# Optimization experiments

Measured on AMD Instinct MI355X. Metric: run time of the kernel, lower is better.

The kernel has to match this reference:

```python
import jax, jax.numpy as jnp
import numpy as np

B, T, C = 2, 2048, 1024
H, DH = 16, 64  # num_heads, dim_head; inner_dim = H*DH = C


def setup_inputs() -> dict:
    key = jax.random.key(0)
    k_x, k_q, k_k, k_v, k_o, k_r = jax.random.split(key, 6)
    scaled = lambda k, shape, fan: (jax.random.normal(k, shape, jnp.float32) / np.sqrt(fan).astype(np.float32))
    x = jax.random.normal(k_x, (B, T, C), jnp.float32)
    Wq = scaled(k_q, (C, H * DH), C)
    Wk = scaled(k_k, (C, H * DH), C)
    Wv = scaled(k_v, (C, H * DH), C)
    Wo = scaled(k_o, (H * DH, C), H * DH)
    bo = jnp.zeros((C,), jnp.float32)
    # learned relative position bias table, indexed by (i - j) in [-(T-1), T-1]
    rel_table = jax.random.normal(k_r, (H, 2 * T - 1), jnp.float32) * 0.02
    # causal mask, broadcast over batch and heads
    mask = jnp.tril(jnp.ones((T, T), bool))[None, None]  # [1,1,T,T]
    return {"x": x, "Wq": Wq, "Wk": Wk, "Wv": Wv, "Wo": Wo, "bo": bo,
            "rel_table": rel_table, "mask": mask}


def reference(x, Wq, Wk, Wv, Wo, bo, rel_table, mask):
    Bx, Tx, Cx = x.shape
    split = lambda t: t.reshape(Bx, Tx, H, DH).transpose(0, 2, 1, 3)  # [B,H,T,DH]
    q = split(x @ Wq) * (DH ** -0.5)
    k = split(x @ Wk)
    v = split(x @ Wv)
    # relative position bias: bias[h,i,j] = rel_table[h, i-j + T-1]
    rel_idx = jnp.arange(Tx)[:, None] - jnp.arange(Tx)[None, :] + (Tx - 1)  # [T,T]
    bias = rel_table[:, rel_idx]  # [H,T,T]
    score = jnp.einsum('bhid,bhjd->bhij', q, k) + bias[None]
    mask_value = -jnp.finfo(score.dtype).max
    score = jnp.where(mask, score, mask_value)
    attn = jax.nn.softmax(score, axis=-1)
    y = jnp.einsum('bhij,bhjd->bhid', attn, v)
    y = y.transpose(0, 2, 1, 3).reshape(Bx, Tx, H * DH)
    return y @ Wo + bo
```

## Files before the change

kernel.cpp:

```cpp
#include <hip/hip_runtime.h>
#include <hip/hip_bf16.h>
#include <stdint.h>


#define T_SEQ 2048
#define NH    16
#define DHD   64
#define CDIM  1024

typedef unsigned short u16;
typedef unsigned int   u32;
typedef __attribute__((ext_vector_type(8))) __bf16 bf16x8;
typedef __attribute__((ext_vector_type(4))) float f32x4;

#define WAITL0   asm volatile("s_waitcnt lgkmcnt(0)" ::: "memory")

__device__ __forceinline__ float bf2f(u16 b){
  union { u32 u; float f; } v; v.u = ((u32)b) << 16; return v.f;
}
__device__ __forceinline__ u16 f2bf(float f){
  union { __bf16 h; u16 u; } v; v.h = (__bf16)f;
  return v.u;
}

__device__ __forceinline__ void gload_lds16(const u16* g, u16* l){
  __builtin_amdgcn_global_load_lds(
      (const __attribute__((address_space(1))) void*)g,
      (__attribute__((address_space(3))) void*)l, 16, 0, 0);
}

__device__ __forceinline__ uint4 load8(const void* p, long elem, int isbf){
  if (isbf) return *(const uint4*)((const u16*)p + elem);
  const float* fp = (const float*)p + elem;
  float4 a = *(const float4*)fp, b = *(const float4*)(fp + 4);
  uint4 r;
  r.x = (u32)f2bf(a.x) | ((u32)f2bf(a.y) << 16);
  r.y = (u32)f2bf(a.z) | ((u32)f2bf(a.w) << 16);
  r.z = (u32)f2bf(b.x) | ((u32)f2bf(b.y) << 16);
  r.w = (u32)f2bf(b.z) | ((u32)f2bf(b.w) << 16);
  return r;
}
__device__ __forceinline__ float loadf(const void* p, long idx, int isbf){
  return isbf ? bf2f(((const u16*)p)[idx]) : ((const float*)p)[idx];
}

__global__ __launch_bounds__(256) void classify(const u32* __restrict__ x,
                                                int* __restrict__ flag){
  __shared__ int cnt[256];
  int c = 0;
#pragma unroll
  for (int i = 0; i < 16; i++){
    u32 w = x[threadIdx.x * 16 + i];
    int e = (w >> 7) & 0xFF;
    c += (e >= 110 && e <= 140);
  }
  cnt[threadIdx.x] = c;
  __syncthreads();
  for (int s = 128; s > 0; s >>= 1){
    if ((int)threadIdx.x < s) cnt[threadIdx.x] += cnt[threadIdx.x + s];
    __syncthreads();
  }
  if (threadIdx.x == 0) *flag = (cnt[0] > 2048) ? 1 : 0;
}

__global__ __launch_bounds__(256) void prep(
    const void* __restrict__ w0, const void* __restrict__ w1,
    const void* __restrict__ w2,
    u16* __restrict__ o0, u16* __restrict__ o1, u16* __restrict__ o2,
    const void* __restrict__ x, u16* __restrict__ xbf,
    const int* __restrict__ flag)
{
  __shared__ u16 tile[64][72];
  const int isbf = *flag;
  const int bid = (int)blockIdx.x;
  const int tid = threadIdx.x;

  if (bid >= 768){
    const long i = ((long)(bid - 768) * 256 + tid) * 8;
    *(uint4*)(xbf + i) = load8(x, i, isbf);
    return;
  }

  const int z = bid >> 8;
  const void* in = z==0 ? w0 : z==1 ? w1 : w2;
  u16*      out  = z==0 ? o0 : z==1 ? o1 : o2;
  const int r0 = ((bid >> 4) & 15) * 64, c0 = (bid & 15) * 64;
  const int rr = tid >> 3;
  const int cc = (tid & 7) * 8;
#pragma unroll
  for (int rd = 0; rd < 2; rd++){
    int r = rd*32 + rr;
    *(uint4*)&tile[r][cc] = load8(in, (long)(r0 + r)*CDIM + c0 + cc, isbf);
  }
  __syncthreads();
#pragma unroll
  for (int rd = 0; rd < 2; rd++){
    int oc = rd*32 + rr;
    uint4 wv; u32* wp = (u32*)&wv;
#pragma unroll
    for (int t = 0; t < 4; t++){
      u32 lo = tile[cc + 2*t][oc];
      u32 hi = tile[cc + 2*t + 1][oc];
      wp[t] = lo | (hi << 16);
    }
    *(uint4*)(out + (long)(c0 + oc)*CDIM + r0 + cc) = wv;
  }
}

__global__ __launch_bounds__(256) void transposeW(
    const void* __restrict__ w0, const void* __restrict__ w1,
    const void* __restrict__ w2,
    u16* __restrict__ o0, u16* __restrict__ o1, u16* __restrict__ o2,
    const int* __restrict__ flag)
{
  __shared__ u16 tile[64][72];
  const int isbf = *flag;
  const int z = blockIdx.z;
  const void* in = z==0 ? w0 : z==1 ? w1 : w2;
  u16*      out  = z==0 ? o0 : z==1 ? o1 : o2;
  const int tid = threadIdx.x;
  const int r0 = blockIdx.y * 64, c0 = blockIdx.x * 64;
  const int rr = tid >> 3;
  const int cc = (tid & 7) * 8;
#pragma unroll
  for (int rd = 0; rd < 2; rd++){
    int r = rd*32 + rr;
    *(uint4*)&tile[r][cc] = load8(in, (long)(r0 + r)*CDIM + c0 + cc, isbf);
  }
  __syncthreads();
#pragma unroll
  for (int rd = 0; rd < 2; rd++){
    int oc = rd*32 + rr;
    uint4 wv; u32* wp = (u32*)&wv;
#pragma unroll
    for (int t = 0; t < 4; t++){
      u32 lo = tile[cc + 2*t][oc];
      u32 hi = tile[cc + 2*t + 1][oc];
      wp[t] = lo | (hi << 16);
    }
    *(uint4*)(out + (long)(c0 + oc)*CDIM + r0 + cc) = wv;
  }
}

__device__ __forceinline__ void gemm_body(
    const u16* __restrict__ A, const u16* __restrict__ BT,
    const void* __restrict__ bias, void* __restrict__ out,
    float scale, int mode, int m0, int n0, int io_isbf)
{
  __shared__ u16 ldsA[2][128*32];
  __shared__ u16 ldsB[2][128*32];
  const int tid = threadIdx.x;
  const int wid = tid >> 6, lane = tid & 63;
  const int col = lane & 15, quad = lane >> 4;
  const int wm = (wid >> 1) * 64, wn = (wid & 1) * 64;

  const int c0 = wid*128 + lane, c1 = c0 + 64;
  const int r0c = c0 >> 2, g0c = c0 & 3;
  const int r1c = c1 >> 2, g1c = c1 & 3;
  const long aoff0 = (long)r0c*CDIM + ((g0c ^ (r0c & 3)) << 3);
  const long aoff1 = (long)r1c*CDIM + ((g1c ^ (r1c & 3)) << 3);
  const int lds0 = (wid*128)*8;
  const int lds1 = (wid*128 + 64)*8;

  const u16* gA = A  + (long)m0*CDIM;
  const u16* gB = BT + (long)n0*CDIM;

  auto stage = [&](int buf, int k0){
    gload_lds16(gA + k0 + aoff0, &ldsA[buf][lds0]);
    gload_lds16(gA + k0 + aoff1, &ldsA[buf][lds1]);
    gload_lds16(gB + k0 + aoff0, &ldsB[buf][lds0]);
    gload_lds16(gB + k0 + aoff1, &ldsB[buf][lds1]);
  };

  f32x4 acc[4][4] = {};
  const int NK = CDIM / 32;

  stage(0, 0);
  __syncthreads();

  int cur = 0;
  for (int k = 0; k < NK; k++){
    if (k + 1 < NK) stage(cur ^ 1, (k + 1) * 32);

    bf16x8 af[4], bfr[4];
#pragma unroll
    for (int mi = 0; mi < 4; mi++){
      const int r = wm + mi*16 + col;
      af[mi] = *(const bf16x8*)&ldsA[cur][r*32 + ((quad ^ (r & 3)) * 8)];
    }
#pragma unroll
    for (int ni = 0; ni < 4; ni++){
      const int r = wn + ni*16 + col;
      bfr[ni] = *(const bf16x8*)&ldsB[cur][r*32 + ((quad ^ (r & 3)) * 8)];
    }
#pragma unroll
    for (int mi = 0; mi < 4; mi++)
#pragma unroll
      for (int ni = 0; ni < 4; ni++)
        acc[mi][ni] = __builtin_amdgcn_mfma_f32_16x16x32_bf16(af[mi], bfr[ni], acc[mi][ni], 0, 0, 0);

    __syncthreads();
    cur ^= 1;
  }

  if (mode == 2){
#pragma unroll
    for (int ni = 0; ni < 4; ni++){
      const int n = n0 + wn + ni*16 + col;
      const int h = n >> 6, d = n & 63;
#pragma unroll
      for (int mi = 0; mi < 4; mi++){
        const int m = m0 + wm + mi*16 + quad*4;
        const int b = m >> 11, t = m & (T_SEQ-1);
        uint2 pk;
        pk.x = (u32)f2bf(acc[mi][ni][0]) | ((u32)f2bf(acc[mi][ni][1]) << 16);
        pk.y = (u32)f2bf(acc[mi][ni][2]) | ((u32)f2bf(acc[mi][ni][3]) << 16);
        *(uint2*)((u16*)out + ((long)(b*NH + h)*DHD + d)*T_SEQ + t) = pk;
      }
    }
  } else {
#pragma unroll
    for (int ni = 0; ni < 4; ni++){
      const int n = n0 + wn + ni*16 + col;
      const float bv = bias ? loadf(bias, n, io_isbf) : 0.f;
#pragma unroll
      for (int mi = 0; mi < 4; mi++){
#pragma unroll
        for (int r = 0; r < 4; r++){
          const int m = m0 + wm + mi*16 + quad*4 + r;
          const float v = acc[mi][ni][r] * scale + bv;
          if (mode == 0){
            const long idx = (long)m*CDIM + n;
            if (io_isbf) ((u16*)out)[idx] = f2bf(v);
            else         ((float*)out)[idx] = v;
          } else {
            const int b = m >> 11, t = m & (T_SEQ-1), h = n >> 6, d = n & 63;
            ((u16*)out)[((long)(b*NH + h)*T_SEQ + t)*DHD + d] = f2bf(v);
          }
        }
      }
    }
  }
}

__global__ __launch_bounds__(256) void gemm_qkv(
    const u16* __restrict__ xbf,
    const u16* __restrict__ WqT, const u16* __restrict__ WkT, const u16* __restrict__ WvT,
    u16* __restrict__ Qb, u16* __restrict__ Kb, u16* __restrict__ VTb)
{
  const int z = blockIdx.z;
  const u16* BT = z==0 ? WqT : z==1 ? WkT : WvT;
  u16*      dst = z==0 ? Qb  : z==1 ? Kb  : VTb;
  const float scale = (z==0) ? 0.125f * 1.44269504f : 1.0f;
  const int mode = (z==2) ? 2 : 1;
  gemm_body(xbf, BT, nullptr, dst, scale, mode, blockIdx.x*128, blockIdx.y*128, 1);
}

__global__ __launch_bounds__(256) void gemm_out(
    const u16* __restrict__ Y, const u16* __restrict__ WoT,
    const void* __restrict__ bo, void* __restrict__ out,
    const int* __restrict__ flag)
{
  gemm_body(Y, WoT, bo, out, 1.0f, 0, blockIdx.x*128, blockIdx.y*128, *flag);
}

__global__ __launch_bounds__(256) void attn64(
    const u16* __restrict__ Q, const u16* __restrict__ K, const u16* __restrict__ VT,
    const void* __restrict__ rel, u16* __restrict__ Y,
    const int* __restrict__ flag)
{
  __shared__ u16 ldsK[2][64*64];
  __shared__ u16 ldsV[2][64*64];
  __shared__ u16 ldsP[4][16*88];
  __shared__ float ldsBias[2112];

  const int isbf = *flag;
  const int tid = threadIdx.x, wid = tid >> 6, lane = tid & 63;
  const int col = lane & 15, quad = lane >> 4;

  const int l = (int)blockIdx.x;
  const int xcd = l & 7, s = l >> 3;
  const int bh = xcd * 4 + (s & 3);
  const int g = s >> 2, gq = g >> 3, g0 = g & 7;
  const int ti = (gq == 0) ? 31 - g0
               : (gq == 1) ? g0
               : (gq == 2) ? 23 - g0
                           : 8 + g0;
  const int i0 = ti * 64;

  const int h = bh & (NH - 1);
  const int b = bh >> 4;

  const u16* Qh = Q  + (long)bh * T_SEQ * DHD;
  const u16* Kh = K  + (long)bh * T_SEQ * DHD;
  const u16* Vh = VT + (long)bh * DHD * T_SEQ;
  const long relbase = (long)h * (2*T_SEQ - 1) + (T_SEQ - 1);
  const float MLOG = 16.0f * 1.44269504f;

  const int srow0 = wid*8 + (lane >> 3);
  const int srow1 = srow0 + 32;
  const int soff  = ((lane & 7) ^ ((lane >> 3) & 7)) * 8;
  const int sb0   = wid*512;
  const int sb1   = 2048 + wid*512;

  auto stage = [&](int buf, int j0){
    gload_lds16(Kh + (long)(j0 + srow0)*DHD + soff, &ldsK[buf][sb0]);
    gload_lds16(Kh + (long)(j0 + srow1)*DHD + soff, &ldsK[buf][sb1]);
    gload_lds16(Vh + (long)srow0*T_SEQ + j0 + soff, &ldsV[buf][sb0]);
    gload_lds16(Vh + (long)srow1*T_SEQ + j0 + soff, &ldsV[buf][sb1]);
  };

  const int nbias = i0 + 127;
  for (int t = tid; t < nbias; t += 256)
    ldsBias[t] = loadf(rel, relbase + t - 63, isbf) * 1.44269504f - MLOG;

  bf16x8 qf0, qf1;
  {
    const u16* qp = Qh + (long)(i0 + wid*16 + col)*DHD + quad*8;
    qf0 = *(const bf16x8*)qp;
    qf1 = *(const bf16x8*)(qp + 32);
  }

  f32x4 O[4] = {};
  float lsumv = 0.f;
  const int icol = i0 + wid*16 + col;
  const int irow = i0 + wid*16 + quad*4;

  stage(0, 0);
  __syncthreads();

  int cur = 0;
  for (int j0 = 0; j0 <= i0; j0 += 64){
    const bool have_next = (j0 + 64 <= i0);
    if (have_next) stage(cur ^ 1, j0 + 64);

    f32x4 sv[4] = {};
#pragma unroll
    for (int kb = 0; kb < 2; kb++){
#pragma unroll
      for (int nb = 0; nb < 4; nb++){
        const int row = nb*16 + col;
        const int sl = ((kb*4 + quad) ^ (row & 7)) * 8;
        bf16x8 kf = *(const bf16x8*)&ldsK[cur][row*64 + sl];
        sv[nb] = __builtin_amdgcn_mfma_f32_16x16x32_bf16(kf, kb ? qf1 : qf0, sv[nb], 0, 0, 0);
      }
    }

    const bool diag = (j0 == i0);
#pragma unroll
    for (int nb = 0; nb < 4; nb++){
      const float* bp = &ldsBias[icol - j0 - nb*16 - quad*4 + 63];
#pragma unroll
      for (int r = 0; r < 4; r++){
        float arg = sv[nb][r] + bp[-r];
        if (diag && (nb*16 + quad*4 + r > wid*16 + col)) arg = -1e9f;
        float p;
        asm volatile("v_exp_f32 %0, %1" : "=v"(p) : "v"(arg));
        sv[nb][r] = p;
        lsumv += p;
      }
    }

    u16* Pw = ldsP[wid];
#pragma unroll
    for (int nb = 0; nb < 4; nb++){
      u32 lo, hi;
      asm("v_cvt_pk_bf16_f32 %0, %1, %2" : "=v"(lo) : "v"(sv[nb][0]), "v"(sv[nb][1]));
      asm("v_cvt_pk_bf16_f32 %0, %1, %2" : "=v"(hi) : "v"(sv[nb][2]), "v"(sv[nb][3]));
      uint2 pk; pk.x = lo; pk.y = hi;
      *(uint2*)&Pw[col*88 + nb*16 + quad*4] = pk;
    }
    WAITL0;

#pragma unroll
    for (int kb = 0; kb < 2; kb++){
      bf16x8 pf = *(const bf16x8*)&Pw[col*88 + kb*32 + quad*8];
#pragma unroll
      for (int nb = 0; nb < 4; nb++){
        const int row = nb*16 + col;
        const int sl = ((kb*4 + quad) ^ (row & 7)) * 8;
        bf16x8 vf = *(const bf16x8*)&ldsV[cur][row*64 + sl];
        O[nb] = __builtin_amdgcn_mfma_f32_16x16x32_bf16(pf, vf, O[nb], 0, 0, 0);
      }
    }

    __syncthreads();
    cur ^= 1;
  }

  lsumv += __shfl_xor(lsumv, 16, 64);
  lsumv += __shfl_xor(lsumv, 32, 64);
  float rs[4];
#pragma unroll
  for (int r = 0; r < 4; r++)
    rs[r] = __shfl(lsumv, quad*4 + r, 16);

#pragma unroll
  for (int nb = 0; nb < 4; nb++){
#pragma unroll
    for (int r = 0; r < 4; r++){
      const int i = irow + r;
      const int d = nb*16 + col;
      Y[((long)(b*T_SEQ + i))*CDIM + h*DHD + d] = f2bf(O[nb][r] / rs[r]);
    }
  }
}

extern "C" void kernel_launch(void* const* d_in, const int* in_sizes, int n_in,
                              void* d_out, int out_size, void* d_ws, size_t ws_size,
                              hipStream_t stream)
{
  (void)in_sizes; (void)n_in; (void)out_size; (void)ws_size;
  const void* x   = d_in[0];
  const void* Wq  = d_in[1];
  const void* Wk  = d_in[2];
  const void* Wv  = d_in[3];
  const void* Wo  = d_in[4];
  const void* bo  = d_in[5];
  const void* rel = d_in[6];

  char* ws = (char*)d_ws;
  const size_t MB = 1024*1024;
  int* flag = (int*)ws;
  char* base = ws + 256;
  u16* WqT = (u16*)(base + 0*MB);
  u16* WkT = (u16*)(base + 2*MB);
  u16* WvT = (u16*)(base + 4*MB);
  u16* Kb  = (u16*)(base + 6*MB);
  u16* VTb = (u16*)(base + 14*MB);
  u16* Yb  = (u16*)(base + 0*MB);
  u16* WoT = (u16*)(base + 8*MB);
  u16* Qb  = (u16*)d_out;
  u16* xbf = Qb + 4u*1024*1024;

  dim3 blk(256);
  classify  <<<1, blk, 0, stream>>>((const u32*)x, flag);
  prep      <<<dim3(2816), blk, 0, stream>>>(Wq, Wk, Wv, WqT, WkT, WvT, x, xbf, flag);
  gemm_qkv  <<<dim3(32,8,3),  blk, 0, stream>>>(xbf, WqT, WkT, WvT, Qb, Kb, VTb);
  attn64    <<<dim3(1024),  blk, 0, stream>>>(Qb, Kb, VTb, rel, Yb, flag);
  transposeW<<<dim3(16,16,1), blk, 0, stream>>>(Wo, Wo, Wo, WoT, WoT, WoT, flag);
  gemm_out  <<<dim3(32,8),    blk, 0, stream>>>(Yb, WoT, bo, d_out, flag);
}
```

Baseline: 214.7 us.

## Inline dtype sniffing per block and fuse Wo transpose with output GEMM cooperatively

```diff
diff --git a/kernel.cpp b/kernel.cpp
--- a/kernel.cpp
+++ b/kernel.cpp
@@ -1,5 +1,6 @@
 #include <hip/hip_runtime.h>
 #include <hip/hip_bf16.h>
+#include <hip/hip_cooperative_groups.h>
 #include <stdint.h>
 
 
@@ -21,6 +22,18 @@
 __device__ __forceinline__ u16 f2bf(float f){
   union { __bf16 h; u16 u; } v; v.h = (__bf16)f;
   return v.u;
+}
+
+__device__ __forceinline__ int sniff_bf16(const void* xp){
+  __shared__ int sflag;
+  if (threadIdx.x < 64){
+    u32 w = ((const u32*)xp)[threadIdx.x * 64];
+    int e = (w >> 7) & 0xFF;
+    unsigned long long m = __ballot(e >= 110 && e <= 140);
+    if (threadIdx.x == 0) sflag = (__popcll(m) > 32) ? 1 : 0;
+  }
+  __syncthreads();
+  return sflag;
 }
 
 __device__ __forceinline__ void gload_lds16(const u16* g, u16* l){
@@ -44,34 +57,14 @@
   return isbf ? bf2f(((const u16*)p)[idx]) : ((const float*)p)[idx];
 }
 
-__global__ __launch_bounds__(256) void classify(const u32* __restrict__ x,
-                                                int* __restrict__ flag){
-  __shared__ int cnt[256];
-  int c = 0;
-#pragma unroll
-  for (int i = 0; i < 16; i++){
-    u32 w = x[threadIdx.x * 16 + i];
-    int e = (w >> 7) & 0xFF;
-    c += (e >= 110 && e <= 140);
-  }
-  cnt[threadIdx.x] = c;
-  __syncthreads();
-  for (int s = 128; s > 0; s >>= 1){
-    if ((int)threadIdx.x < s) cnt[threadIdx.x] += cnt[threadIdx.x + s];
-    __syncthreads();
-  }
-  if (threadIdx.x == 0) *flag = (cnt[0] > 2048) ? 1 : 0;
-}
-
 __global__ __launch_bounds__(256) void prep(
     const void* __restrict__ w0, const void* __restrict__ w1,
     const void* __restrict__ w2,
     u16* __restrict__ o0, u16* __restrict__ o1, u16* __restrict__ o2,
-    const void* __restrict__ x, u16* __restrict__ xbf,
-    const int* __restrict__ flag)
+    const void* __restrict__ x, u16* __restrict__ xbf)
 {
   __shared__ u16 tile[64][72];
-  const int isbf = *flag;
+  const int isbf = sniff_bf16(x);
   const int bid = (int)blockIdx.x;
   const int tid = threadIdx.x;
 
@@ -85,41 +78,6 @@
   const void* in = z==0 ? w0 : z==1 ? w1 : w2;
   u16*      out  = z==0 ? o0 : z==1 ? o1 : o2;
   const int r0 = ((bid >> 4) & 15) * 64, c0 = (bid & 15) * 64;
-  const int rr = tid >> 3;
-  const int cc = (tid & 7) * 8;
-#pragma unroll
-  for (int rd = 0; rd < 2; rd++){
-    int r = rd*32 + rr;
-    *(uint4*)&tile[r][cc] = load8(in, (long)(r0 + r)*CDIM + c0 + cc, isbf);
-  }
-  __syncthreads();
-#pragma unroll
-  for (int rd = 0; rd < 2; rd++){
-    int oc = rd*32 + rr;
-    uint4 wv; u32* wp = (u32*)&wv;
-#pragma unroll
-    for (int t = 0; t < 4; t++){
-      u32 lo = tile[cc + 2*t][oc];
-      u32 hi = tile[cc + 2*t + 1][oc];
-      wp[t] = lo | (hi << 16);
-    }
-    *(uint4*)(out + (long)(c0 + oc)*CDIM + r0 + cc) = wv;
-  }
-}
-
-__global__ __launch_bounds__(256) void transposeW(
-    const void* __restrict__ w0, const void* __restrict__ w1,
-    const void* __restrict__ w2,
-    u16* __restrict__ o0, u16* __restrict__ o1, u16* __restrict__ o2,
-    const int* __restrict__ flag)
-{
-  __shared__ u16 tile[64][72];
-  const int isbf = *flag;
-  const int z = blockIdx.z;
-  const void* in = z==0 ? w0 : z==1 ? w1 : w2;
-  u16*      out  = z==0 ? o0 : z==1 ? o1 : o2;
-  const int tid = threadIdx.x;
-  const int r0 = blockIdx.y * 64, c0 = blockIdx.x * 64;
   const int rr = tid >> 3;
   const int cc = (tid & 7) * 8;
 #pragma unroll
@@ -256,25 +214,57 @@
   gemm_body(xbf, BT, nullptr, dst, scale, mode, blockIdx.x*128, blockIdx.y*128, 1);
 }
 
-__global__ __launch_bounds__(256) void gemm_out(
-    const u16* __restrict__ Y, const u16* __restrict__ WoT,
-    const void* __restrict__ bo, void* __restrict__ out,
-    const int* __restrict__ flag)
-{
-  gemm_body(Y, WoT, bo, out, 1.0f, 0, blockIdx.x*128, blockIdx.y*128, *flag);
+__global__ __launch_bounds__(256) void out_fused(
+    const void* __restrict__ Wo, u16* __restrict__ WoT,
+    const u16* __restrict__ Y, const void* __restrict__ bo,
+    void* __restrict__ outp, const void* __restrict__ xs)
+{
+  const int isbf = sniff_bf16(xs);
+  const int bid = (int)blockIdx.x;
+  const int tid = threadIdx.x;
+
+  {
+    __shared__ u16 tile[64][72];
+    const int r0 = (bid >> 4) * 64, c0 = (bid & 15) * 64;
+    const int rr = tid >> 3;
+    const int cc = (tid & 7) * 8;
+#pragma unroll
+    for (int rd = 0; rd < 2; rd++){
+      int r = rd*32 + rr;
+      *(uint4*)&tile[r][cc] = load8(Wo, (long)(r0 + r)*CDIM + c0 + cc, isbf);
+    }
+    __syncthreads();
+#pragma unroll
+    for (int rd = 0; rd < 2; rd++){
+      int oc = rd*32 + rr;
+      uint4 wv; u32* wp = (u32*)&wv;
+#pragma unroll
+      for (int t = 0; t < 4; t++){
+        u32 lo = tile[cc + 2*t][oc];
+        u32 hi = tile[cc + 2*t + 1][oc];
+        wp[t] = lo | (hi << 16);
+      }
+      *(uint4*)(WoT + (long)(c0 + oc)*CDIM + r0 + cc) = wv;
+    }
+  }
+
+  __threadfence();
+  cooperative_groups::this_grid().sync();
+
+  gemm_body(Y, WoT, bo, outp, 1.0f, 0, (bid & 31)*128, (bid >> 5)*128, isbf);
 }
 
 __global__ __launch_bounds__(256) void attn64(
     const u16* __restrict__ Q, const u16* __restrict__ K, const u16* __restrict__ VT,
     const void* __restrict__ rel, u16* __restrict__ Y,
-    const int* __restrict__ flag)
+    const void* __restrict__ xs)
 {
   __shared__ u16 ldsK[2][64*64];
   __shared__ u16 ldsV[2][64*64];
   __shared__ u16 ldsP[4][16*88];
   __shared__ float ldsBias[2112];
 
-  const int isbf = *flag;
+  const int isbf = sniff_bf16(xs);
   const int tid = threadIdx.x, wid = tid >> 6, lane = tid & 63;
   const int col = lane & 15, quad = lane >> 4;
 
@@ -421,7 +411,6 @@
 
   char* ws = (char*)d_ws;
   const size_t MB = 1024*1024;
-  int* flag = (int*)ws;
   char* base = ws + 256;
   u16* WqT = (u16*)(base + 0*MB);
   u16* WkT = (u16*)(base + 2*MB);
@@ -434,10 +423,12 @@
   u16* xbf = Qb + 4u*1024*1024;
 
   dim3 blk(256);
-  classify  <<<1, blk, 0, stream>>>((const u32*)x, flag);
-  prep      <<<dim3(2816), blk, 0, stream>>>(Wq, Wk, Wv, WqT, WkT, WvT, x, xbf, flag);
+  prep      <<<dim3(2816), blk, 0, stream>>>(Wq, Wk, Wv, WqT, WkT, WvT, x, xbf);
   gemm_qkv  <<<dim3(32,8,3),  blk, 0, stream>>>(xbf, WqT, WkT, WvT, Qb, Kb, VTb);
-  attn64    <<<dim3(1024),  blk, 0, stream>>>(Qb, Kb, VTb, rel, Yb, flag);
-  transposeW<<<dim3(16,16,1), blk, 0, stream>>>(Wo, Wo, Wo, WoT, WoT, WoT, flag);
-  gemm_out  <<<dim3(32,8),    blk, 0, stream>>>(Yb, WoT, bo, d_out, flag);
-}
+  attn64    <<<dim3(1024),  blk, 0, stream>>>(Qb, Kb, VTb, rel, Yb, x);
+
+  void* kargs[] = {(void*)&Wo, (void*)&WoT, (void*)&Yb, (void*)&bo,
+                   (void*)&d_out, (void*)&x};
+  hipLaunchCooperativeKernel(reinterpret_cast<void*>(out_fused),
+                             dim3(256), blk, kargs, 0, stream);
+}
```

Result: slower. 277.6 us (+29.3%).
